# Kernel optimization log

Measured on AMD Instinct MI355X. Metric: run time of the kernel, lower is better.

## Reference

```python
import jax, jax.numpy as jnp
import numpy as np

N_NODES = 50000
N_EDGES = 1600000
IN_CH = 128
HEADS = 4
HEAD_DIM = 32  # out_channels // heads = 128 // 4
NEG_SLOPE = 0.2


def setup_inputs() -> dict:
    key = jax.random.key(0)
    ks = jax.random.split(key, 6)
    x = jax.random.normal(ks[0], (N_NODES, IN_CH), dtype=jnp.float32)
    edge_index = jax.random.randint(ks[1], (2, N_EDGES), 0, N_NODES, dtype=jnp.int64)
    W = jax.random.normal(ks[2], (IN_CH, HEADS * HEAD_DIM), dtype=jnp.float32) * 0.1
    att_src = jax.random.normal(ks[3], (HEADS, HEAD_DIM), dtype=jnp.float32) * 0.1
    att_dst = jax.random.normal(ks[4], (HEADS, HEAD_DIM), dtype=jnp.float32) * 0.1
    bias = jax.random.normal(ks[5], (HEADS * HEAD_DIM,), dtype=jnp.float32) * 0.1
    return {"x": x, "edge_index": edge_index, "W": W,
            "att_src": att_src, "att_dst": att_dst, "bias": bias}


def reference(x, edge_index, W, att_src, att_dst, bias):
    N = x.shape[0]
    # linear projection, split heads: [N, H, C]
    h = (x @ W).reshape(N, HEADS, HEAD_DIM)
    # per-node attention logits: [N, H]
    a_src = jnp.einsum('nhc,hc->nh', h, att_src)
    a_dst = jnp.einsum('nhc,hc->nh', h, att_dst)
    # add self loops (PyG default)
    loops = jnp.arange(N, dtype=edge_index.dtype)
    src = jnp.concatenate([edge_index[0], loops])  # message source j
    dst = jnp.concatenate([edge_index[1], loops])  # message target i
    # edge attention scores: [E_total, H]
    alpha = jax.nn.leaky_relu(a_src[src] + a_dst[dst], NEG_SLOPE)
    # segment softmax over incoming edges per destination node
    amax = jax.ops.segment_max(alpha, dst, num_segments=N)
    alpha = jnp.exp(alpha - amax[dst])
    denom = jax.ops.segment_sum(alpha, dst, num_segments=N)
    alpha = alpha / (denom[dst] + 1e-16)
    # weighted scatter-aggregate: [N, H, C]
    msg = h[src] * alpha[:, :, None]
    out = jax.ops.segment_sum(msg, dst, num_segments=N)
    out = out.reshape(N, HEADS * HEAD_DIM) + bias
    return jax.nn.elu(out)
```

## Files before the change

kernel.cpp:

```cpp
#include <hip/hip_runtime.h>

typedef unsigned short u16;
typedef unsigned int u32;

#define CH 128
#define NHEAD 4
#define NEG_SLOPE 0.2f
#define ROWS_PER_BLOCK 32

#define NPB 128
#define NBMAX 400
#define BCAP 6144
#define GPAD 16
#define BINA_BLOCKS 256

static __device__ __forceinline__ float bitf(u32 i) {
    float f; __builtin_memcpy(&f, &i, 4); return f;
}
static __device__ __forceinline__ float bflo(u32 v) { return bitf(v << 16); }
static __device__ __forceinline__ float bfhi(u32 v) { return bitf(v & 0xffff0000u); }
static __device__ __forceinline__ u16 f2bf(float f) {
    u32 i; __builtin_memcpy(&i, &f, 4);
    return (u16)((i + 0x7fffu + ((i >> 16) & 1u)) >> 16);
}
static __device__ __forceinline__ float lrelu(float v) { return v > 0.f ? v : NEG_SLOPE * v; }

static __device__ __forceinline__ int ei_at(const int* __restrict__ ei, int mode32, size_t idx) {
    return mode32 ? ei[idx] : ei[2 * idx];
}

__global__ __launch_bounds__(256) void gemmbin_kernel(
    const float* __restrict__ x, const float* __restrict__ W,
    const float* __restrict__ att_src, const float* __restrict__ att_dst,
    u16* __restrict__ h, float* __restrict__ asrc, float* __restrict__ adst, int N,
    const int* __restrict__ ei, int* __restrict__ gcur, u32* __restrict__ rec,
    int E, int NB)
{
    __shared__ float xs[ROWS_PER_BLOCK][CH];
    __shared__ u32 Wbf[CH][CH / 2];
    __shared__ int hist[NBMAX];
    __shared__ int hbase[NBMAX];
    __shared__ int hcur[NBMAX];

    const int tid = threadIdx.x;

    if (blockIdx.x < BINA_BLOCKS) {
        const int mode32 = __syncthreads_or(ei[2 * tid + 1] != 0);
        for (int b = tid; b < NB; b += 256) { hist[b] = 0; hcur[b] = 0; }
        __syncthreads();
        const int chunk = (E + BINA_BLOCKS - 1) / BINA_BLOCKS;
        const int beg0 = blockIdx.x * chunk;
        const int end0 = min(E, beg0 + chunk);
#pragma unroll 4
        for (int e = beg0 + tid; e < end0; e += 256) {
            int dj = ei_at(ei, mode32, (size_t)E + e);
            atomicAdd(&hist[dj >> 7], 1);
        }
        __syncthreads();
        for (int b = tid; b < NB; b += 256) {
            int c = hist[b];
            hbase[b] = c ? atomicAdd(&gcur[b * GPAD], c) : 0;
        }
        __syncthreads();
#pragma unroll 4
        for (int e = beg0 + tid; e < end0; e += 256) {
            int dj = ei_at(ei, mode32, (size_t)E + e);
            int sj = ei_at(ei, mode32, (size_t)e);
            int bkt = dj >> 7;
            int r = atomicAdd(&hcur[bkt], 1);
            int pos = hbase[bkt] + r;
            if (pos < BCAP)
                rec[(size_t)bkt * BCAP + pos] = ((u32)sj << 7) | (u32)(dj & 127);
        }
        return;
    }

    const int gb = blockIdx.x - BINA_BLOCKS;
    const int r0b = gb * ROWS_PER_BLOCK;
    {
#pragma unroll
        for (int i = 0; i < 16; ++i) {
            int f = tid + i * 256;
            int row = f >> 5;
            int col = (f & 31) * 4;
            float4 w4 = *(const float4*)(W + (size_t)row * CH + col);
            Wbf[row][(col >> 1)]     = (u32)f2bf(w4.x) | ((u32)f2bf(w4.y) << 16);
            Wbf[row][(col >> 1) + 1] = (u32)f2bf(w4.z) | ((u32)f2bf(w4.w) << 16);
        }
#pragma unroll
        for (int i = 0; i < 4; ++i) {
            int f = tid + i * 256;
            int row = f >> 5;
            int col = (f & 31) * 4;
            if (r0b + row < N)
                *(float4*)&xs[row][col] = *(const float4*)(x + (size_t)(r0b + row) * CH + col);
        }
    }
    __syncthreads();

    const int lane = tid & 63;
    const int wave = tid >> 6;
    const int c0 = lane * 2;
    const int head = lane >> 4;
    const float as0 = att_src[c0], as1 = att_src[c0 + 1];
    const float ad0 = att_dst[c0], ad1 = att_dst[c0 + 1];
    const int rw = wave * 8;

    float acc[8][2];
#pragma unroll
    for (int r = 0; r < 8; ++r) { acc[r][0] = 0.f; acc[r][1] = 0.f; }

#pragma unroll 4
    for (int k4 = 0; k4 < 32; ++k4) {
        const int k = k4 * 4;
        u32 p0 = Wbf[k + 0][lane];
        u32 p1 = Wbf[k + 1][lane];
        u32 p2 = Wbf[k + 2][lane];
        u32 p3 = Wbf[k + 3][lane];
        float w00 = bflo(p0), w01 = bfhi(p0);
        float w10 = bflo(p1), w11 = bfhi(p1);
        float w20 = bflo(p2), w21 = bfhi(p2);
        float w30 = bflo(p3), w31 = bfhi(p3);
#pragma unroll
        for (int r = 0; r < 8; ++r) {
            float4 xv = *(const float4*)&xs[rw + r][k];
            acc[r][0] = fmaf(xv.x, w00, acc[r][0]);
            acc[r][1] = fmaf(xv.x, w01, acc[r][1]);
            acc[r][0] = fmaf(xv.y, w10, acc[r][0]);
            acc[r][1] = fmaf(xv.y, w11, acc[r][1]);
            acc[r][0] = fmaf(xv.z, w20, acc[r][0]);
            acc[r][1] = fmaf(xv.z, w21, acc[r][1]);
            acc[r][0] = fmaf(xv.w, w30, acc[r][0]);
            acc[r][1] = fmaf(xv.w, w31, acc[r][1]);
        }
    }
#pragma unroll
    for (int r = 0; r < 8; ++r) {
        int row = r0b + rw + r;
        float sdot = acc[r][0] * as0 + acc[r][1] * as1;
        float ddot = acc[r][0] * ad0 + acc[r][1] * ad1;
#pragma unroll
        for (int o = 1; o < 16; o <<= 1) {
            sdot += __shfl_xor(sdot, o, 64);
            ddot += __shfl_xor(ddot, o, 64);
        }
        if (row < N) {
            u32 hp = (u32)f2bf(acc[r][0]) | ((u32)f2bf(acc[r][1]) << 16);
            *(u32*)(h + (size_t)row * CH + c0) = hp;
            if ((lane & 15) == 0) {
                asrc[row * NHEAD + head] = sdot;
                adst[row * NHEAD + head] = ddot;
            }
        }
    }
}

__global__ __launch_bounds__(256) void binB_kernel(
    const int* __restrict__ gcur, const u32* __restrict__ rec,
    int* __restrict__ csr, int* __restrict__ begA, int* __restrict__ degA, int N)
{
    __shared__ u32 recs[BCAP];
    __shared__ int lcnt[NPB];
    __shared__ int lsc[NPB];
    __shared__ int lcur[NPB];
    const int tid = threadIdx.x;
    const int bkt = blockIdx.x;
    int cnt0 = gcur[bkt * GPAD];
    cnt0 = cnt0 < BCAP ? cnt0 : BCAP;
    const size_t rbase = (size_t)bkt * BCAP;

    if (tid < NPB) { lcnt[tid] = 0; lcur[tid] = 0; }
    for (int i = tid; i < cnt0; i += 256) recs[i] = rec[rbase + i];
    __syncthreads();
#pragma unroll 4
    for (int i = tid; i < cnt0; i += 256) atomicAdd(&lcnt[recs[i] & 127], 1);
    __syncthreads();
    if (tid < NPB) lsc[tid] = lcnt[tid];
    __syncthreads();
    for (int o = 1; o < NPB; o <<= 1) {
        int v = (tid < NPB && tid >= o) ? lsc[tid - o] : 0;
        __syncthreads();
        if (tid < NPB) lsc[tid] += v;
        __syncthreads();
    }
#pragma unroll 4
    for (int i = tid; i < cnt0; i += 256) {
        u32 rc = recs[i];
        int local = rc & 127;
        int r = atomicAdd(&lcur[local], 1);
        int slot = (lsc[local] - lcnt[local]) + r;
        csr[rbase + slot] = (int)(rc >> 7);
    }
    if (tid < NPB) {
        int node = (bkt << 7) + tid;
        if (node < N) {
            begA[node] = (int)rbase + (lsc[tid] - lcnt[tid]);
            degA[node] = lcnt[tid];
        }
    }
}

__global__ __launch_bounds__(256) void agg_kernel(
    const u16* __restrict__ h, const float* __restrict__ asrc, const float* __restrict__ adst,
    const int* __restrict__ begA, const int* __restrict__ degA, const int* __restrict__ csr,
    const float* __restrict__ bias, float* __restrict__ out, int N)
{
    const int lane = threadIdx.x & 63;
    const int wave = threadIdx.x >> 6;
    const int node = blockIdx.x * 4 + wave;
    if (node >= N) return;
    const int g = lane >> 4;
    const int l = lane & 15;
    const int c8 = l * 8;
    const int head = l >> 2;
    const int beg = begA[node];
    const int end = beg + degA[node];
    const float4 ad4 = *(const float4*)(adst + node * 4);
    const float adh = (head == 0) ? ad4.x : (head == 1) ? ad4.y : (head == 2) ? ad4.z : ad4.w;

    const float4 asl = *(const float4*)(asrc + node * 4);
    float mx0 = lrelu(asl.x + ad4.x);
    float mx1 = lrelu(asl.y + ad4.y);
    float mx2 = lrelu(asl.z + ad4.z);
    float mx3 = lrelu(asl.w + ad4.w);
    for (int e = beg + lane; e < end; e += 64) {
        int j = csr[e];
        float4 a = *(const float4*)(asrc + j * 4);
        mx0 = fmaxf(mx0, lrelu(a.x + ad4.x));
        mx1 = fmaxf(mx1, lrelu(a.y + ad4.y));
        mx2 = fmaxf(mx2, lrelu(a.z + ad4.z));
        mx3 = fmaxf(mx3, lrelu(a.w + ad4.w));
    }
#pragma unroll
    for (int o = 1; o < 64; o <<= 1) {
        mx0 = fmaxf(mx0, __shfl_xor(mx0, o, 64));
        mx1 = fmaxf(mx1, __shfl_xor(mx1, o, 64));
        mx2 = fmaxf(mx2, __shfl_xor(mx2, o, 64));
        mx3 = fmaxf(mx3, __shfl_xor(mx3, o, 64));
    }
    const float mh = (head == 0) ? mx0 : (head == 1) ? mx1 : (head == 2) ? mx2 : mx3;

    float acc[8];
#pragma unroll
    for (int k = 0; k < 8; ++k) acc[k] = 0.f;
    float s = 0.f;

    int e = beg + g;
    if (e < end) {
        int j0 = csr[e];
        int j1 = csr[e + 4];
        bool v1 = (e + 4) < end;
        j0 = ((u32)j0 < (u32)N) ? j0 : 0;
        j1 = ((u32)j1 < (u32)N) ? j1 : 0;
        float a0 = asrc[j0 * NHEAD + head];
        float a1 = asrc[j1 * NHEAD + head];
        a1 = v1 ? a1 : -1e30f;
        uint4 h0 = *(const uint4*)(h + (size_t)j0 * CH + c8);
        uint4 h1 = *(const uint4*)(h + (size_t)j1 * CH + c8);
        for (;;) {
            const int ep = e + 8;
            bool vp0 = ep < end;
            bool vp1 = (ep + 4) < end;
            int jp0 = csr[ep];
            int jp1 = csr[ep + 4];
            jp0 = ((u32)jp0 < (u32)N) ? jp0 : 0;
            jp1 = ((u32)jp1 < (u32)N) ? jp1 : 0;
            float ap0 = asrc[jp0 * NHEAD + head];
            float ap1 = asrc[jp1 * NHEAD + head];
            ap0 = vp0 ? ap0 : -1e30f;
            ap1 = vp1 ? ap1 : -1e30f;
            uint4 hp0 = *(const uint4*)(h + (size_t)jp0 * CH + c8);
            uint4 hp1 = *(const uint4*)(h + (size_t)jp1 * CH + c8);

            float w0 = __expf(lrelu(a0 + adh) - mh);
            float w1 = __expf(lrelu(a1 + adh) - mh);
            s += w0 + w1;
            acc[0] = fmaf(w0, bflo(h0.x), acc[0]);
            acc[1] = fmaf(w0, bfhi(h0.x), acc[1]);
            acc[2] = fmaf(w0, bflo(h0.y), acc[2]);
            acc[3] = fmaf(w0, bfhi(h0.y), acc[3]);
            acc[4] = fmaf(w0, bflo(h0.z), acc[4]);
            acc[5] = fmaf(w0, bfhi(h0.z), acc[5]);
            acc[6] = fmaf(w0, bflo(h0.w), acc[6]);
            acc[7] = fmaf(w0, bfhi(h0.w), acc[7]);
            acc[0] = fmaf(w1, bflo(h1.x), acc[0]);
            acc[1] = fmaf(w1, bfhi(h1.x), acc[1]);
            acc[2] = fmaf(w1, bflo(h1.y), acc[2]);
            acc[3] = fmaf(w1, bfhi(h1.y), acc[3]);
            acc[4] = fmaf(w1, bflo(h1.z), acc[4]);
            acc[5] = fmaf(w1, bfhi(h1.z), acc[5]);
            acc[6] = fmaf(w1, bflo(h1.w), acc[6]);
            acc[7] = fmaf(w1, bfhi(h1.w), acc[7]);

            a0 = ap0; a1 = ap1; h0 = hp0; h1 = hp1; e = ep;
            if (e >= end) break;
        }
    }
    if (g == 0) {
        float aslh = (head == 0) ? asl.x : (head == 1) ? asl.y : (head == 2) ? asl.z : asl.w;
        float w = __expf(lrelu(aslh + adh) - mh);
        s += w;
        uint4 hv = *(const uint4*)(h + (size_t)node * CH + c8);
        acc[0] = fmaf(w, bflo(hv.x), acc[0]);
        acc[1] = fmaf(w, bfhi(hv.x), acc[1]);
        acc[2] = fmaf(w, bflo(hv.y), acc[2]);
        acc[3] = fmaf(w, bfhi(hv.y), acc[3]);
        acc[4] = fmaf(w, bflo(hv.z), acc[4]);
        acc[5] = fmaf(w, bfhi(hv.z), acc[5]);
        acc[6] = fmaf(w, bflo(hv.w), acc[6]);
        acc[7] = fmaf(w, bfhi(hv.w), acc[7]);
    }
#pragma unroll
    for (int o = 16; o < 64; o <<= 1) {
        s += __shfl_xor(s, o, 64);
#pragma unroll
        for (int k = 0; k < 8; ++k) acc[k] += __shfl_xor(acc[k], o, 64);
    }
    if (g == 0) {
        const float inv = 1.f / (s + 1e-16f);
        float o0[8];
#pragma unroll
        for (int k = 0; k < 8; ++k) {
            float v = acc[k] * inv + bias[c8 + k];
            o0[k] = v > 0.f ? v : __expf(v) - 1.f;
        }
        float4 lo = make_float4(o0[0], o0[1], o0[2], o0[3]);
        float4 hi = make_float4(o0[4], o0[5], o0[6], o0[7]);
        *(float4*)(out + (size_t)node * CH + c8) = lo;
        *(float4*)(out + (size_t)node * CH + c8 + 4) = hi;
    }
}

extern "C" void kernel_launch(void* const* d_in, const int* in_sizes, int n_in,
                              void* d_out, int out_size, void* d_ws, size_t ws_size,
                              hipStream_t stream)
{
    const float* x       = (const float*)d_in[0];
    const int*   ei      = (const int*)d_in[1];
    const float* W       = (const float*)d_in[2];
    const float* att_src = (const float*)d_in[3];
    const float* att_dst = (const float*)d_in[4];
    const float* bias    = (const float*)d_in[5];
    float* out = (float*)d_out;
    const int N = in_sizes[0] / CH;
    const int E = in_sizes[1] / 2;
    const int NB = (N + NPB - 1) / NPB;

    char* p = (char*)d_ws;
    auto alloc = [&](size_t bytes) { char* r = p; p += (bytes + 255) & ~(size_t)255; return r; };
    u16*   h    = (u16*)alloc((size_t)N * CH * 2);
    float* asrc = (float*)alloc((size_t)N * NHEAD * 4);
    float* adst = (float*)alloc((size_t)N * NHEAD * 4);
    int*   gcur = (int*)alloc((size_t)NB * GPAD * 4);
    u32*   rec  = (u32*)alloc((size_t)NB * BCAP * 4);
    int*   csr  = (int*)alloc((size_t)NB * BCAP * 4 + 256);
    int*   begA = (int*)alloc((size_t)N * 4);
    int*   degA = (int*)alloc((size_t)N * 4);

    const int gemmBlocks = (N + ROWS_PER_BLOCK - 1) / ROWS_PER_BLOCK;
    hipMemsetAsync(gcur, 0, (size_t)NB * GPAD * 4, stream);
    gemmbin_kernel<<<BINA_BLOCKS + gemmBlocks, 256, 0, stream>>>(
        x, W, att_src, att_dst, h, asrc, adst, N, ei, gcur, rec, E, NB);
    binB_kernel<<<NB, 256, 0, stream>>>(gcur, rec, csr, begA, degA, N);
    agg_kernel<<<(N + 3) / 4, 256, 0, stream>>>(h, asrc, adst, begA, degA, csr, bias, out, N);
}
```

Before: 217.7 us.

## Halve bucket size and stage CSR scatter in shared memory for coalesced writes

Buckets now hold 64 nodes instead of 128, which doubles the bucket count (up to 832) and halves per-bucket capacity to 3072. In binB, records are held in registers (up to 12 per thread) instead of a shared staging array. The scatter into sorted order goes to a shared output buffer, which is then copied to global memory with coalesced stores. This is meant to remove uncoalesced global scatter writes and give more blocks for parallelism, at the cost of more atomic contention in the histogram and a tighter overflow cap per bucket.

```diff
diff --git a/kernel.cpp b/kernel.cpp
--- a/kernel.cpp
+++ b/kernel.cpp
@@ -8,9 +8,11 @@
 #define NEG_SLOPE 0.2f
 #define ROWS_PER_BLOCK 32
 
-#define NPB 128
-#define NBMAX 400
-#define BCAP 6144
+#define LOG_NPB 6
+#define NPB 64
+#define NBMAX 832
+#define BCAP 3072
+#define KMAX 12
 #define GPAD 16
 #define BINA_BLOCKS 256
 
@@ -54,7 +56,7 @@
 #pragma unroll 4
         for (int e = beg0 + tid; e < end0; e += 256) {
             int dj = ei_at(ei, mode32, (size_t)E + e);
-            atomicAdd(&hist[dj >> 7], 1);
+            atomicAdd(&hist[dj >> LOG_NPB], 1);
         }
         __syncthreads();
         for (int b = tid; b < NB; b += 256) {
@@ -66,11 +68,11 @@
         for (int e = beg0 + tid; e < end0; e += 256) {
             int dj = ei_at(ei, mode32, (size_t)E + e);
             int sj = ei_at(ei, mode32, (size_t)e);
-            int bkt = dj >> 7;
+            int bkt = dj >> LOG_NPB;
             int r = atomicAdd(&hcur[bkt], 1);
             int pos = hbase[bkt] + r;
             if (pos < BCAP)
-                rec[(size_t)bkt * BCAP + pos] = ((u32)sj << 7) | (u32)(dj & 127);
+                rec[(size_t)bkt * BCAP + pos] = ((u32)sj << LOG_NPB) | (u32)(dj & (NPB - 1));
         }
         return;
     }
@@ -159,7 +161,7 @@
     const int* __restrict__ gcur, const u32* __restrict__ rec,
     int* __restrict__ csr, int* __restrict__ begA, int* __restrict__ degA, int N)
 {
-    __shared__ u32 recs[BCAP];
+    __shared__ int outb[BCAP];
     __shared__ int lcnt[NPB];
     __shared__ int lsc[NPB];
     __shared__ int lcur[NPB];
@@ -170,10 +172,17 @@
     const size_t rbase = (size_t)bkt * BCAP;
 
     if (tid < NPB) { lcnt[tid] = 0; lcur[tid] = 0; }
-    for (int i = tid; i < cnt0; i += 256) recs[i] = rec[rbase + i];
-    __syncthreads();
-#pragma unroll 4
-    for (int i = tid; i < cnt0; i += 256) atomicAdd(&lcnt[recs[i] & 127], 1);
+
+    u32 rc[KMAX];
+#pragma unroll
+    for (int k = 0; k < KMAX; ++k) {
+        int i = tid + k * 256;
+        rc[k] = (i < cnt0) ? rec[rbase + i] : 0xffffffffu;
+    }
+    __syncthreads();
+#pragma unroll
+    for (int k = 0; k < KMAX; ++k)
+        if (rc[k] != 0xffffffffu) atomicAdd(&lcnt[rc[k] & (NPB - 1)], 1);
     __syncthreads();
     if (tid < NPB) lsc[tid] = lcnt[tid];
     __syncthreads();
@@ -183,16 +192,20 @@
         if (tid < NPB) lsc[tid] += v;
         __syncthreads();
     }
-#pragma unroll 4
-    for (int i = tid; i < cnt0; i += 256) {
-        u32 rc = recs[i];
-        int local = rc & 127;
-        int r = atomicAdd(&lcur[local], 1);
-        int slot = (lsc[local] - lcnt[local]) + r;
-        csr[rbase + slot] = (int)(rc >> 7);
-    }
+#pragma unroll
+    for (int k = 0; k < KMAX; ++k) {
+        if (rc[k] != 0xffffffffu) {
+            int local = rc[k] & (NPB - 1);
+            int r = atomicAdd(&lcur[local], 1);
+            int slot = (lsc[local] - lcnt[local]) + r;
+            outb[slot] = (int)(rc[k] >> LOG_NPB);
+        }
+    }
+    __syncthreads();
+    for (int i = tid; i < cnt0; i += 256)
+        csr[rbase + i] = outb[i];
     if (tid < NPB) {
-        int node = (bkt << 7) + tid;
+        int node = (bkt << LOG_NPB) + tid;
         if (node < N) {
             begA[node] = (int)rbase + (lsc[tid] - lcnt[tid]);
             degA[node] = lcnt[tid];
```

Result: no change. 219.7 us (+0.9%).
